# Optimization experiments

Hardware: AMD Instinct MI355X
Metric: run time of the kernel (lower is better)

Reference implementation:

```python
import jax, jax.numpy as jnp
import numpy as np

C_T, C_Z, C_HID, N_HEADS = 64, 128, 16, 4
N_TEMPL, N_RES = 4, 512
INF = 1e9


def setup_inputs() -> dict:
    key = jax.random.key(0)
    ks = jax.random.split(key, 7)
    return {
        "t": jax.random.normal(ks[0], (N_TEMPL, N_RES, N_RES, C_T), jnp.float32),
        "z": jax.random.normal(ks[1], (N_RES, N_RES, C_Z), jnp.float32),
        "template_mask": jnp.ones((N_TEMPL,), jnp.float32),
        "wq": jax.random.normal(ks[2], (C_Z, N_HEADS * C_HID), jnp.float32) * 0.05,
        "wk": jax.random.normal(ks[3], (C_T, N_HEADS * C_HID), jnp.float32) * 0.05,
        "wv": jax.random.normal(ks[4], (C_T, N_HEADS * C_HID), jnp.float32) * 0.05,
        "wo": jax.random.normal(ks[5], (N_HEADS * C_HID, C_Z), jnp.float32) * 0.05,
        "bo": jnp.zeros((C_Z,), jnp.float32),
    }


def reference(t, z, template_mask, wq, wk, wv, wo, bo):
    # t: [S, N, N, C_t]  z: [N, N, C_z]  template_mask: [S]
    h, d = N_HEADS, C_HID
    bias = INF * (template_mask - 1.0)  # [S], 0 for kept, -inf for masked
    tp = jnp.transpose(t, (1, 2, 0, 3))  # [N, N, S, C_t] (permute_final_dims (1,2,0,3))
    scale = 1.0 / jnp.sqrt(jnp.asarray(d, z.dtype))
    q = jnp.einsum("ijc,chd->ijhd", z, wq.reshape(C_Z, h, d)) * scale  # [N,N,h,d]
    k = jnp.einsum("ijsc,chd->ijshd", tp, wk.reshape(C_T, h, d))       # [N,N,S,h,d]
    v = jnp.einsum("ijsc,chd->ijshd", tp, wv.reshape(C_T, h, d))
    logits = jnp.einsum("ijhd,ijshd->ijhs", q, k) + bias  # [N,N,h,S]
    a = jax.nn.softmax(logits, axis=-1)
    o = jnp.einsum("ijhs,ijshd->ijhd", a, v).reshape(N_RES, N_RES, h * d)
    out = o @ wo + bo  # [N, N, C_z]
    out = out * (jnp.sum(template_mask) > 0).astype(out.dtype)
    return out
```

## Files before the change

### kernel.cpp

```cpp
#include <hip/hip_runtime.h>
#include <hip/hip_bf16.h>

#define NRES 512
#define CZ   128
#define CT   64

typedef short bf16x8 __attribute__((ext_vector_type(8)));
typedef float f32x4  __attribute__((ext_vector_type(4)));

#define MFMA16(a,b,c) __builtin_amdgcn_mfma_f32_16x16x32_bf16((a),(b),(c),0,0,0)

__device__ __forceinline__ unsigned short f2bf(float f){
  __hip_bfloat16 h = __float2bfloat16(f);
  return __builtin_bit_cast(unsigned short, h);
}
__device__ __forceinline__ bf16x8 pack8(const float4 a, const float4 b){
  bf16x8 r;
  r[0]=(short)f2bf(a.x); r[1]=(short)f2bf(a.y); r[2]=(short)f2bf(a.z); r[3]=(short)f2bf(a.w);
  r[4]=(short)f2bf(b.x); r[5]=(short)f2bf(b.y); r[6]=(short)f2bf(b.z); r[7]=(short)f2bf(b.w);
  return r;
}

template<int CTRL>
__device__ __forceinline__ float dppadd(float x){
  int y = __builtin_amdgcn_update_dpp(0, __builtin_bit_cast(int, x), CTRL, 0xF, 0xF, false);
  return x + __builtin_bit_cast(float, y);
}
__device__ __forceinline__ f32x4 reduce16(f32x4 p){
#pragma unroll
  for (int r = 0; r < 4; ++r){
    float v = p[r];
    v = dppadd<0xB1>(v);
    v = dppadd<0x4E>(v);
    v = dppadd<0x141>(v);
    v = dppadd<0x140>(v);
    p[r] = v;
  }
  return p;
}

__global__ void prep_pack(const float* __restrict__ wq, const float* __restrict__ wk,
                          const float* __restrict__ wv, const float* __restrict__ wo,
                          unsigned short* __restrict__ packed){
  int idx = blockIdx.x * 256 + threadIdx.x;
  if (idx >= 48 * 64) return;
  int f = idx >> 6, lane = idx & 63;
  const float* W; int Ncols, nt, ks; float scale = 1.0f;
  if (f < 16)      { W = wq; Ncols = 64;  nt = f >> 2;        ks = f & 3;        scale = 0.25f; }
  else if (f < 24) { W = wk; Ncols = 64;  nt = (f - 16) >> 1; ks = (f - 16) & 1; }
  else if (f < 32) { W = wv; Ncols = 64;  nt = (f - 24) >> 1; ks = (f - 24) & 1; }
  else             { W = wo; Ncols = 128; nt = (f - 32) >> 1; ks = (f - 32) & 1; }
  int col = nt * 16 + (lane & 15);
  int k0  = ks * 32 + (lane >> 4) * 8;
  unsigned short* dst = packed + (size_t)f * 512 + (size_t)lane * 8;
#pragma unroll
  for (int j = 0; j < 8; ++j)
    dst[j] = f2bf(W[(k0 + j) * Ncols + col] * scale);
}

__launch_bounds__(256, 3)
__global__ void tpa_main(const float* __restrict__ t, const float* __restrict__ z,
                         const float* __restrict__ mask, const float* __restrict__ bo,
                         const unsigned short* __restrict__ packed,
                         float* __restrict__ out){
  __shared__ __align__(16) char smem[49152];

  const int tid  = threadIdx.x;
  const int lane = tid & 63;
  const int w    = tid >> 6;
  const int cl   = lane & 15;
  const int g    = lane >> 4;
  const int b    = blockIdx.x;
  const int i    = b >> 3;
  const int j0   = (b & 7) << 6;
  const int r0   = j0 + (w << 4);
  const int grow = r0 + cl;

#pragma unroll
  for (int it = 0; it < 12; ++it){
    int idx = it * 256 + tid;
    __builtin_amdgcn_global_load_lds(
        reinterpret_cast<const uint4*>(packed) + idx,
        reinterpret_cast<uint4*>(smem) + idx, 16, 0, 0);
  }

  const float4* zp = reinterpret_cast<const float4*>(z + ((size_t)i * NRES + grow) * CZ);
  bf16x8 za[4];
#pragma unroll
  for (int ks = 0; ks < 4; ++ks){
    float4 p0 = zp[ks * 8 + g * 2 + 0];
    float4 p1 = zp[ks * 8 + g * 2 + 1];
    za[ks] = pack8(p0, p1);
  }

  bf16x8 ta[4][2];
#pragma unroll
  for (int s = 0; s < 4; ++s){
    const float4* tp4 = reinterpret_cast<const float4*>(
        t + (((size_t)s * NRES + i) * NRES + grow) * CT);
    float4 a0 = tp4[g * 2 + 0];
    float4 a1 = tp4[g * 2 + 1];
    float4 a2 = tp4[8 + g * 2 + 0];
    float4 a3 = tp4[8 + g * 2 + 1];
    ta[s][0] = pack8(a0, a1);
    ta[s][1] = pack8(a2, a3);
  }

  float m0 = mask[0], m1 = mask[1], m2 = mask[2], m3 = mask[3];
  float msum = m0 + m1 + m2 + m3;
  float bias[4] = {1e9f * (m0 - 1.0f), 1e9f * (m1 - 1.0f),
                   1e9f * (m2 - 1.0f), 1e9f * (m3 - 1.0f)};

  __syncthreads();

#define LDB(fi) (*reinterpret_cast<const bf16x8*>(smem + (size_t)(fi) * 1024 + (size_t)lane * 16))

  f32x4 qf[4];
#pragma unroll
  for (int h = 0; h < 4; ++h){
    f32x4 q = {0.f, 0.f, 0.f, 0.f};
#pragma unroll
    for (int ks = 0; ks < 4; ++ks) q = MFMA16(za[ks], LDB(h * 4 + ks), q);
    qf[h] = q;
  }

  __syncthreads();

  unsigned short* o_ws = reinterpret_cast<unsigned short*>(smem + w * 2048);

#pragma unroll
  for (int h = 0; h < 4; ++h){
    f32x4 lgh[4];
#pragma unroll
    for (int s = 0; s < 4; ++s){
      f32x4 acc = {0.f, 0.f, 0.f, 0.f};
      acc = MFMA16(ta[s][0], LDB(16 + h * 2 + 0), acc);
      acc = MFMA16(ta[s][1], LDB(16 + h * 2 + 1), acc);
      f32x4 p = reduce16(acc * qf[h]);
#pragma unroll
      for (int r = 0; r < 4; ++r) p[r] += bias[s];
      lgh[s] = p;
    }
    f32x4 mx, sum = {0.f, 0.f, 0.f, 0.f};
#pragma unroll
    for (int r = 0; r < 4; ++r)
      mx[r] = fmaxf(fmaxf(lgh[0][r], lgh[1][r]), fmaxf(lgh[2][r], lgh[3][r]));
#pragma unroll
    for (int s = 0; s < 4; ++s){
#pragma unroll
      for (int r = 0; r < 4; ++r) lgh[s][r] = __expf(lgh[s][r] - mx[r]);
      sum += lgh[s];
    }
    f32x4 inv;
#pragma unroll
    for (int r = 0; r < 4; ++r) inv[r] = 1.0f / sum[r];
#pragma unroll
    for (int s = 0; s < 4; ++s) lgh[s] *= inv;

    f32x4 of = {0.f, 0.f, 0.f, 0.f};
#pragma unroll
    for (int s = 0; s < 4; ++s){
      f32x4 vacc = {0.f, 0.f, 0.f, 0.f};
      vacc = MFMA16(ta[s][0], LDB(24 + h * 2 + 0), vacc);
      vacc = MFMA16(ta[s][1], LDB(24 + h * 2 + 1), vacc);
      of += lgh[s] * vacc;
    }
#pragma unroll
    for (int r = 0; r < 4; ++r){
      int row = (g << 2) + r;
      o_ws[row * 64 + ((h * 16 + cl) ^ ((row & 7) << 3))] = (unsigned short)f2bf(of[r]);
    }
  }
  asm volatile("s_waitcnt lgkmcnt(0)" ::: "memory");

  {
    bf16x8 oa[2];
#pragma unroll
    for (int ks = 0; ks < 2; ++ks)
      oa[ks] = *reinterpret_cast<const bf16x8*>(
          o_ws + cl * 64 + ((ks * 32 + g * 8) ^ ((cl & 7) << 3)));

    float gate = (msum > 0.0f) ? 1.0f : 0.0f;
    float* outg = out + ((size_t)i * NRES + r0) * CZ;
#pragma unroll
    for (int nt = 0; nt < 8; ++nt){
      f32x4 acc = {0.f, 0.f, 0.f, 0.f};
      acc = MFMA16(oa[0], LDB(32 + nt * 2 + 0), acc);
      acc = MFMA16(oa[1], LDB(32 + nt * 2 + 1), acc);
      int col = nt * 16 + cl;
      float bov = bo[col];
#pragma unroll
      for (int r = 0; r < 4; ++r)
        outg[(size_t)((g << 2) + r) * CZ + col] = (acc[r] + bov) * gate;
    }
  }
}

extern "C" void kernel_launch(void* const* d_in, const int* in_sizes, int n_in,
                              void* d_out, int out_size, void* d_ws, size_t ws_size,
                              hipStream_t stream) {
  const float* t    = (const float*)d_in[0];
  const float* z    = (const float*)d_in[1];
  const float* mask = (const float*)d_in[2];
  const float* wq   = (const float*)d_in[3];
  const float* wk   = (const float*)d_in[4];
  const float* wv   = (const float*)d_in[5];
  const float* wo   = (const float*)d_in[6];
  const float* bo   = (const float*)d_in[7];
  unsigned short* packed = (unsigned short*)d_ws;

  hipLaunchKernelGGL(prep_pack, dim3(12), dim3(256), 0, stream, wq, wk, wv, wo, packed);
  hipLaunchKernelGGL(tpa_main, dim3(4096), dim3(256), 0, stream,
                     t, z, mask, bo, packed, (float*)d_out);
}
```

Baseline: 111.9 us.

## Use 1024-thread blocks sharing LDS weights and a padded per-wave output scratch

Result: slower. 221.5 us (+97.9%).

```diff
diff --git a/kernel.cpp b/kernel.cpp
--- a/kernel.cpp
+++ b/kernel.cpp
@@ -58,12 +58,13 @@
     dst[j] = f2bf(W[(k0 + j) * Ncols + col] * scale);
 }
 
-__launch_bounds__(256, 3)
+#define WLDS 49152
+__launch_bounds__(1024, 8)
 __global__ void tpa_main(const float* __restrict__ t, const float* __restrict__ z,
                          const float* __restrict__ mask, const float* __restrict__ bo,
                          const unsigned short* __restrict__ packed,
                          float* __restrict__ out){
-  __shared__ __align__(16) char smem[49152];
+  __shared__ __align__(16) char smem[69632];
 
   const int tid  = threadIdx.x;
   const int lane = tid & 63;
@@ -71,14 +72,14 @@
   const int cl   = lane & 15;
   const int g    = lane >> 4;
   const int b    = blockIdx.x;
-  const int i    = b >> 3;
-  const int j0   = (b & 7) << 6;
-  const int r0   = j0 + (w << 4);
+  const int i    = b >> 1;
+  const int jb   = (b & 1) << 8;
+  const int r0   = jb + (w << 4);
   const int grow = r0 + cl;
 
 #pragma unroll
-  for (int it = 0; it < 12; ++it){
-    int idx = it * 256 + tid;
+  for (int it = 0; it < 3; ++it){
+    int idx = it * 1024 + tid;
     __builtin_amdgcn_global_load_lds(
         reinterpret_cast<const uint4*>(packed) + idx,
         reinterpret_cast<uint4*>(smem) + idx, 16, 0, 0);
@@ -106,10 +107,11 @@
     ta[s][1] = pack8(a2, a3);
   }
 
-  float m0 = mask[0], m1 = mask[1], m2 = mask[2], m3 = mask[3];
-  float msum = m0 + m1 + m2 + m3;
-  float bias[4] = {1e9f * (m0 - 1.0f), 1e9f * (m1 - 1.0f),
-                   1e9f * (m2 - 1.0f), 1e9f * (m3 - 1.0f)};
+  const float m0 = mask[0], m1 = mask[1], m2 = mask[2], m3 = mask[3];
+  const float msum = m0 + m1 + m2 + m3;
+  const float gate = (msum > 0.0f) ? 1.0f : 0.0f;
+  const float bias[4] = {1e9f * (m0 - 1.0f), 1e9f * (m1 - 1.0f),
+                         1e9f * (m2 - 1.0f), 1e9f * (m3 - 1.0f)};
 
   __syncthreads();
 
@@ -124,10 +126,9 @@
     qf[h] = q;
   }
 
-  __syncthreads();
-
-  unsigned short* o_ws = reinterpret_cast<unsigned short*>(smem + w * 2048);
-
+  unsigned short* oh = reinterpret_cast<unsigned short*>(smem + WLDS + w * 1280);
+
+  bf16x8 oa0, oa1;
 #pragma unroll
   for (int h = 0; h < 4; ++h){
     f32x4 lgh[4];
@@ -165,28 +166,26 @@
       vacc = MFMA16(ta[s][1], LDB(24 + h * 2 + 1), vacc);
       of += lgh[s] * vacc;
     }
-#pragma unroll
-    for (int r = 0; r < 4; ++r){
-      int row = (g << 2) + r;
-      o_ws[row * 64 + ((h * 16 + cl) ^ ((row & 7) << 3))] = (unsigned short)f2bf(of[r]);
+    const int h2 = h & 1;
+#pragma unroll
+    for (int r = 0; r < 4; ++r)
+      oh[(g * 4 + r) * 40 + h2 * 16 + cl] = f2bf(of[r]);
+    if (h == 1){
+      asm volatile("s_waitcnt lgkmcnt(0)" ::: "memory");
+      oa0 = *reinterpret_cast<const bf16x8*>(oh + cl * 40 + g * 8);
+      asm volatile("s_waitcnt lgkmcnt(0)" ::: "memory");
     }
   }
   asm volatile("s_waitcnt lgkmcnt(0)" ::: "memory");
+  oa1 = *reinterpret_cast<const bf16x8*>(oh + cl * 40 + g * 8);
 
   {
-    bf16x8 oa[2];
-#pragma unroll
-    for (int ks = 0; ks < 2; ++ks)
-      oa[ks] = *reinterpret_cast<const bf16x8*>(
-          o_ws + cl * 64 + ((ks * 32 + g * 8) ^ ((cl & 7) << 3)));
-
-    float gate = (msum > 0.0f) ? 1.0f : 0.0f;
     float* outg = out + ((size_t)i * NRES + r0) * CZ;
 #pragma unroll
     for (int nt = 0; nt < 8; ++nt){
       f32x4 acc = {0.f, 0.f, 0.f, 0.f};
-      acc = MFMA16(oa[0], LDB(32 + nt * 2 + 0), acc);
-      acc = MFMA16(oa[1], LDB(32 + nt * 2 + 1), acc);
+      acc = MFMA16(oa0, LDB(32 + nt * 2 + 0), acc);
+      acc = MFMA16(oa1, LDB(32 + nt * 2 + 1), acc);
       int col = nt * 16 + cl;
       float bov = bo[col];
 #pragma unroll
@@ -210,6 +209,6 @@
   unsigned short* packed = (unsigned short*)d_ws;
 
   hipLaunchKernelGGL(prep_pack, dim3(12), dim3(256), 0, stream, wq, wk, wv, wo, packed);
-  hipLaunchKernelGGL(tpa_main, dim3(4096), dim3(256), 0, stream,
+  hipLaunchKernelGGL(tpa_main, dim3(1024), dim3(1024), 0, stream,
                      t, z, mask, bo, packed, (float*)d_out);
 }
```

## Make main kernel persistent with double-buffered LDS staging of template tiles

Applied to the files above, without the earlier changes.

New measurement: 155.9 us. 39.3% more time.

```diff
diff --git a/kernel.cpp b/kernel.cpp
--- a/kernel.cpp
+++ b/kernel.cpp
@@ -58,12 +58,32 @@
     dst[j] = f2bf(W[(k0 + j) * Ncols + col] * scale);
 }
 
-__launch_bounds__(256, 3)
-__global__ void tpa_main(const float* __restrict__ t, const float* __restrict__ z,
-                         const float* __restrict__ mask, const float* __restrict__ bo,
-                         const unsigned short* __restrict__ packed,
-                         float* __restrict__ out){
-  __shared__ __align__(16) char smem[49152];
+__device__ __forceinline__ void stage_tile(const float* __restrict__ t, char* smem,
+                                           int buf, int tk, int tid){
+  const int i  = tk >> 4;
+  const int j0 = (tk & 15) << 5;
+#pragma unroll
+  for (int s = 0; s < 4; ++s){
+    const float* slab = t + (((size_t)s * NRES + i) * NRES + j0) * CT;
+    char* dstbase = smem + buf * 32768 + s * 8192;
+#pragma unroll
+    for (int it = 0; it < 4; ++it){
+      int c   = it * 128 + tid;
+      int row = c >> 4, col = c & 15;
+      const float* src = slab + row * 64 + ((col ^ (row & 7)) << 2);
+      __builtin_amdgcn_global_load_lds(reinterpret_cast<const uint4*>(src),
+                                       reinterpret_cast<uint4*>(dstbase + (c << 4)),
+                                       16, 0, 0);
+    }
+  }
+}
+
+__global__ void __launch_bounds__(128, 1)
+tpa_main(const float* __restrict__ t, const float* __restrict__ z,
+         const float* __restrict__ mask, const float* __restrict__ bo,
+         const unsigned short* __restrict__ packed,
+         float* __restrict__ out){
+  __shared__ __align__(16) char smem[69632];
 
   const int tid  = threadIdx.x;
   const int lane = tid & 63;
@@ -71,127 +91,142 @@
   const int cl   = lane & 15;
   const int g    = lane >> 4;
   const int b    = blockIdx.x;
-  const int i    = b >> 3;
-  const int j0   = (b & 7) << 6;
-  const int r0   = j0 + (w << 4);
-  const int grow = r0 + cl;
-
-#pragma unroll
-  for (int it = 0; it < 12; ++it){
-    int idx = it * 256 + tid;
-    __builtin_amdgcn_global_load_lds(
-        reinterpret_cast<const uint4*>(packed) + idx,
-        reinterpret_cast<uint4*>(smem) + idx, 16, 0, 0);
-  }
-
-  const float4* zp = reinterpret_cast<const float4*>(z + ((size_t)i * NRES + grow) * CZ);
-  bf16x8 za[4];
-#pragma unroll
-  for (int ks = 0; ks < 4; ++ks){
-    float4 p0 = zp[ks * 8 + g * 2 + 0];
-    float4 p1 = zp[ks * 8 + g * 2 + 1];
-    za[ks] = pack8(p0, p1);
-  }
-
-  bf16x8 ta[4][2];
-#pragma unroll
-  for (int s = 0; s < 4; ++s){
-    const float4* tp4 = reinterpret_cast<const float4*>(
-        t + (((size_t)s * NRES + i) * NRES + grow) * CT);
-    float4 a0 = tp4[g * 2 + 0];
-    float4 a1 = tp4[g * 2 + 1];
-    float4 a2 = tp4[8 + g * 2 + 0];
-    float4 a3 = tp4[8 + g * 2 + 1];
-    ta[s][0] = pack8(a0, a1);
-    ta[s][1] = pack8(a2, a3);
-  }
-
-  float m0 = mask[0], m1 = mask[1], m2 = mask[2], m3 = mask[3];
-  float msum = m0 + m1 + m2 + m3;
-  float bias[4] = {1e9f * (m0 - 1.0f), 1e9f * (m1 - 1.0f),
-                   1e9f * (m2 - 1.0f), 1e9f * (m3 - 1.0f)};
-
-  __syncthreads();
-
-#define LDB(fi) (*reinterpret_cast<const bf16x8*>(smem + (size_t)(fi) * 1024 + (size_t)lane * 16))
-
-  f32x4 qf[4];
-#pragma unroll
-  for (int h = 0; h < 4; ++h){
-    f32x4 q = {0.f, 0.f, 0.f, 0.f};
-#pragma unroll
-    for (int ks = 0; ks < 4; ++ks) q = MFMA16(za[ks], LDB(h * 4 + ks), q);
-    qf[h] = q;
-  }
-
-  __syncthreads();
-
-  unsigned short* o_ws = reinterpret_cast<unsigned short*>(smem + w * 2048);
-
-#pragma unroll
-  for (int h = 0; h < 4; ++h){
-    f32x4 lgh[4];
+
+  stage_tile(t, smem, 0, b * 16 + 0, tid);
+
+  bf16x8 wqr[16], wkr[8], wvr[8], wor[16];
+#pragma unroll
+  for (int f = 0; f < 16; ++f)
+    wqr[f] = *reinterpret_cast<const bf16x8*>(packed + (size_t)f * 512 + (size_t)lane * 8);
+#pragma unroll
+  for (int f = 0; f < 8; ++f)
+    wkr[f] = *reinterpret_cast<const bf16x8*>(packed + (size_t)(16 + f) * 512 + (size_t)lane * 8);
+#pragma unroll
+  for (int f = 0; f < 8; ++f)
+    wvr[f] = *reinterpret_cast<const bf16x8*>(packed + (size_t)(24 + f) * 512 + (size_t)lane * 8);
+#pragma unroll
+  for (int f = 0; f < 16; ++f)
+    wor[f] = *reinterpret_cast<const bf16x8*>(packed + (size_t)(32 + f) * 512 + (size_t)lane * 8);
+
+  const float m0 = mask[0], m1 = mask[1], m2 = mask[2], m3 = mask[3];
+  const float msum = m0 + m1 + m2 + m3;
+  const float gate = (msum > 0.0f) ? 1.0f : 0.0f;
+  const float bias[4] = {1e9f * (m0 - 1.0f), 1e9f * (m1 - 1.0f),
+                         1e9f * (m2 - 1.0f), 1e9f * (m3 - 1.0f)};
+  float bov[8];
+#pragma unroll
+  for (int nt = 0; nt < 8; ++nt) bov[nt] = bo[nt * 16 + cl];
+
+  unsigned short* o_ws = reinterpret_cast<unsigned short*>(smem + 65536 + w * 2048);
+  const int rowi = w * 16 + cl;
+  const int rs   = rowi & 7;
+
+#pragma unroll 1
+  for (int k = 0; k < 16; ++k){
+    const int cur = k & 1;
+    __syncthreads();
+
+    const int tk = b * 16 + k;
+    const int i  = tk >> 4;
+    const int j0 = (tk & 15) << 5;
+    const int grow = j0 + rowi;
+
+    const float4* zp = reinterpret_cast<const float4*>(z + ((size_t)i * NRES + grow) * CZ);
+    float4 zr[8];
+#pragma unroll
+    for (int ks = 0; ks < 4; ++ks){
+      zr[ks * 2 + 0] = zp[ks * 8 + g * 2 + 0];
+      zr[ks * 2 + 1] = zp[ks * 8 + g * 2 + 1];
+    }
+
+    if (k < 15) stage_tile(t, smem, cur ^ 1, tk + 1, tid);
+
+    bf16x8 ta[4][2];
 #pragma unroll
     for (int s = 0; s < 4; ++s){
-      f32x4 acc = {0.f, 0.f, 0.f, 0.f};
-      acc = MFMA16(ta[s][0], LDB(16 + h * 2 + 0), acc);
-      acc = MFMA16(ta[s][1], LDB(16 + h * 2 + 1), acc);
-      f32x4 p = reduce16(acc * qf[h]);
-#pragma unroll
-      for (int r = 0; r < 4; ++r) p[r] += bias[s];
-      lgh[s] = p;
-    }
-    f32x4 mx, sum = {0.f, 0.f, 0.f, 0.f};
-#pragma unroll
-    for (int r = 0; r < 4; ++r)
-      mx[r] = fmaxf(fmaxf(lgh[0][r], lgh[1][r]), fmaxf(lgh[2][r], lgh[3][r]));
-#pragma unroll
-    for (int s = 0; s < 4; ++s){
-#pragma unroll
-      for (int r = 0; r < 4; ++r) lgh[s][r] = __expf(lgh[s][r] - mx[r]);
-      sum += lgh[s];
-    }
-    f32x4 inv;
-#pragma unroll
-    for (int r = 0; r < 4; ++r) inv[r] = 1.0f / sum[r];
-#pragma unroll
-    for (int s = 0; s < 4; ++s) lgh[s] *= inv;
-
-    f32x4 of = {0.f, 0.f, 0.f, 0.f};
-#pragma unroll
-    for (int s = 0; s < 4; ++s){
-      f32x4 vacc = {0.f, 0.f, 0.f, 0.f};
-      vacc = MFMA16(ta[s][0], LDB(24 + h * 2 + 0), vacc);
-      vacc = MFMA16(ta[s][1], LDB(24 + h * 2 + 1), vacc);
-      of += lgh[s] * vacc;
-    }
-#pragma unroll
-    for (int r = 0; r < 4; ++r){
-      int row = (g << 2) + r;
-      o_ws[row * 64 + ((h * 16 + cl) ^ ((row & 7) << 3))] = (unsigned short)f2bf(of[r]);
-    }
-  }
-  asm volatile("s_waitcnt lgkmcnt(0)" ::: "memory");
-
-  {
+      const char* base = smem + cur * 32768 + s * 8192 + rowi * 256;
+#pragma unroll
+      for (int ks = 0; ks < 2; ++ks){
+        int c0 = ks * 8 + g * 2;
+        float4 lo = *reinterpret_cast<const float4*>(base + ((c0 ^ rs) << 4));
+        float4 hi = *reinterpret_cast<const float4*>(base + (((c0 + 1) ^ rs) << 4));
+        ta[s][ks] = pack8(lo, hi);
+      }
+    }
+    bf16x8 za[4];
+#pragma unroll
+    for (int ks = 0; ks < 4; ++ks) za[ks] = pack8(zr[ks * 2], zr[ks * 2 + 1]);
+
+    f32x4 qf[4];
+#pragma unroll
+    for (int h = 0; h < 4; ++h){
+      f32x4 q = {0.f, 0.f, 0.f, 0.f};
+#pragma unroll
+      for (int ks = 0; ks < 4; ++ks) q = MFMA16(za[ks], wqr[h * 4 + ks], q);
+      qf[h] = q;
+    }
+
+#pragma unroll
+    for (int h = 0; h < 4; ++h){
+      f32x4 lgh[4];
+#pragma unroll
+      for (int s = 0; s < 4; ++s){
+        f32x4 acc = {0.f, 0.f, 0.f, 0.f};
+        acc = MFMA16(ta[s][0], wkr[h * 2 + 0], acc);
+        acc = MFMA16(ta[s][1], wkr[h * 2 + 1], acc);
+        f32x4 p = reduce16(acc * qf[h]);
+#pragma unroll
+        for (int r = 0; r < 4; ++r) p[r] += bias[s];
+        lgh[s] = p;
+      }
+      f32x4 mx, sum = {0.f, 0.f, 0.f, 0.f};
+#pragma unroll
+      for (int r = 0; r < 4; ++r)
+        mx[r] = fmaxf(fmaxf(lgh[0][r], lgh[1][r]), fmaxf(lgh[2][r], lgh[3][r]));
+#pragma unroll
+      for (int s = 0; s < 4; ++s){
+#pragma unroll
+        for (int r = 0; r < 4; ++r) lgh[s][r] = __expf(lgh[s][r] - mx[r]);
+        sum += lgh[s];
+      }
+      f32x4 inv;
+#pragma unroll
+      for (int r = 0; r < 4; ++r) inv[r] = 1.0f / sum[r];
+#pragma unroll
+      for (int s = 0; s < 4; ++s) lgh[s] *= inv;
+
+      f32x4 of = {0.f, 0.f, 0.f, 0.f};
+#pragma unroll
+      for (int s = 0; s < 4; ++s){
+        f32x4 vacc = {0.f, 0.f, 0.f, 0.f};
+        vacc = MFMA16(ta[s][0], wvr[h * 2 + 0], vacc);
+        vacc = MFMA16(ta[s][1], wvr[h * 2 + 1], vacc);
+        of += lgh[s] * vacc;
+      }
+#pragma unroll
+      for (int r = 0; r < 4; ++r){
+        int row = (g << 2) + r;
+        o_ws[row * 64 + ((h * 16 + cl) ^ ((row & 7) << 3))] = (unsigned short)f2bf(of[r]);
+      }
+    }
+    asm volatile("s_waitcnt lgkmcnt(0)" ::: "memory");
+
     bf16x8 oa[2];
 #pragma unroll
     for (int ks = 0; ks < 2; ++ks)
       oa[ks] = *reinterpret_cast<const bf16x8*>(
           o_ws + cl * 64 + ((ks * 32 + g * 8) ^ ((cl & 7) << 3)));
 
-    float gate = (msum > 0.0f) ? 1.0f : 0.0f;
-    float* outg = out + ((size_t)i * NRES + r0) * CZ;
+    float* outg = out + ((size_t)i * NRES + j0 + (w << 4)) * CZ;
 #pragma unroll
     for (int nt = 0; nt < 8; ++nt){
       f32x4 acc = {0.f, 0.f, 0.f, 0.f};
-      acc = MFMA16(oa[0], LDB(32 + nt * 2 + 0), acc);
-      acc = MFMA16(oa[1], LDB(32 + nt * 2 + 1), acc);
+      acc = MFMA16(oa[0], wor[nt * 2 + 0], acc);
+      acc = MFMA16(oa[1], wor[nt * 2 + 1], acc);
       int col = nt * 16 + cl;
-      float bov = bo[col];
 #pragma unroll
       for (int r = 0; r < 4; ++r)
-        outg[(size_t)((g << 2) + r) * CZ + col] = (acc[r] + bov) * gate;
+        outg[(size_t)((g << 2) + r) * CZ + col] = (acc[r] + bov[nt]) * gate;
     }
   }
 }
@@ -210,6 +245,6 @@
   unsigned short* packed = (unsigned short*)d_ws;
 
   hipLaunchKernelGGL(prep_pack, dim3(12), dim3(256), 0, stream, wq, wk, wv, wo, packed);
-  hipLaunchKernelGGL(tpa_main, dim3(4096), dim3(256), 0, stream,
+  hipLaunchKernelGGL(tpa_main, dim3(512), dim3(128), 0, stream,
                      t, z, mask, bo, packed, (float*)d_out);
 }
```
